# Optimization experiments

Hardware: AMD Instinct MI355X
Metric: run time of the kernel (lower is better)

Reference implementation:

```python
import jax, jax.numpy as jnp
import numpy as np
import math

B, S, E, H = 2, 2048, 1024, 16
D = E // H  # d_head = 64

def setup_inputs() -> dict:
    key = jax.random.key(0)
    ks = jax.random.split(key, 7)
    query = jax.random.normal(ks[0], (B, S, E), dtype=jnp.float32)
    k_in = jax.random.normal(ks[1], (B, S, E), dtype=jnp.float32)
    v_in = jax.random.normal(ks[2], (B, S, E), dtype=jnp.float32)
    # causal mask, broadcastable over batch and heads; mask==0 positions are blocked
    mask = jnp.tril(jnp.ones((S, S), dtype=jnp.int32))[None, None]
    scale = 1.0 / math.sqrt(E)
    w_q = jax.random.normal(ks[3], (E, E), dtype=jnp.float32) * scale
    w_k = jax.random.normal(ks[4], (E, E), dtype=jnp.float32) * scale
    w_v = jax.random.normal(ks[5], (E, E), dtype=jnp.float32) * scale
    w_o = jax.random.normal(ks[6], (E, E), dtype=jnp.float32) * scale
    return {"query": query, "key": k_in, "value": v_in, "mask": mask,
            "w_q": w_q, "w_k": w_k, "w_v": w_v, "w_o": w_o}

def reference(query, key, value, mask, w_q, w_k, w_v, w_o):
    # projections (nn.Linear with no bias: x @ W^T); split heads -> [B,H,S,D]
    q = (query @ w_q.T).reshape(B, S, H, D).transpose(0, 2, 1, 3)
    k = (key @ w_k.T).reshape(B, S, H, D).transpose(0, 2, 1, 3)
    v = (value @ w_v.T).reshape(B, S, H, D).transpose(0, 2, 1, 3)
    # scaled dot-product scores [B,H,S,S]
    scores = jnp.einsum('bhqd,bhkd->bhqk', q, k) / math.sqrt(D)
    scores = jnp.where(mask == 0, jnp.float32(-1e9), scores)
    attn = jax.nn.softmax(scores, axis=-1)  # dropout p=0.0 -> identity
    out = jnp.einsum('bhqk,bhkd->bhqd', attn, v)  # [B,H,S,D]
    out = out.transpose(0, 2, 1, 3).reshape(B, S, E)
    return out @ w_o.T
```

## Files before the change

### kernel.cpp

```cpp
#include <hip/hip_runtime.h>
#include <hip/hip_bf16.h>

#define B_ 2
#define S_ 2048
#define E_ 1024
#define H_ 16
#define D_ 64

typedef __attribute__((ext_vector_type(8))) short bf16x8;
typedef __attribute__((ext_vector_type(4))) float f32x4;

static __device__ __forceinline__ unsigned short f2bf(float x) {
    union { float f; unsigned u; } v; v.f = x;
    unsigned r = v.u + 0x7FFF + ((v.u >> 16) & 1);
    return (unsigned short)(r >> 16);
}

static __device__ __forceinline__ unsigned pack2bf(float a, float b) {
    union { float f; unsigned u; } x, y; x.f = a; y.f = b;
    unsigned ra = x.u + 0x7FFF + ((x.u >> 16) & 1);
    unsigned rb = y.u + 0x7FFF + ((y.u >> 16) & 1);
    return (ra >> 16) | (rb & 0xFFFF0000u);
}

static __device__ __forceinline__ unsigned packtrunc(float a, float b) {
    union { float f; unsigned u; } x, y; x.f = a; y.f = b;
    return __builtin_amdgcn_perm(y.u, x.u, 0x07060302);
}

static __device__ __forceinline__ void async_copy16(const void* gsrc, void* ldst) {
    __builtin_amdgcn_global_load_lds(
        (const __attribute__((address_space(1))) void*)gsrc,
        (__attribute__((address_space(3))) void*)ldst, 16, 0, 0);
}

__global__ void cvt_all(const float* __restrict__ s0, const float* __restrict__ s1,
                        const float* __restrict__ s2, const float* __restrict__ s3,
                        const float* __restrict__ s4, const float* __restrict__ s5,
                        const float* __restrict__ s6,
                        unsigned short* __restrict__ xdst, unsigned short* __restrict__ wdst,
                        float scq) {
    int b = blockIdx.x;
    const float* src; unsigned short* dst; int i; float c = 1.f;
    if (b < 12288) {
        int ti = b >> 12, lb = b & 4095;
        src = (ti == 0) ? s0 : (ti == 1) ? s1 : s2;
        dst = xdst + (size_t)ti * 4194304;
        i = lb * 256 + threadIdx.x;
    } else {
        int r = b - 12288, ti = r >> 10, lb = r & 1023;
        src = (ti == 0) ? s3 : (ti == 1) ? s4 : (ti == 2) ? s5 : s6;
        dst = wdst + (size_t)ti * 1048576;
        i = lb * 256 + threadIdx.x;
        if (ti == 0) c = scq;
    }
    float4 f = ((const float4*)src)[i];
    ushort4 o;
    o.x = f2bf(f.x * c); o.y = f2bf(f.y * c); o.z = f2bf(f.z * c); o.w = f2bf(f.w * c);
    ((ushort4*)dst)[i] = o;
}

template <int MODE>
__global__ __launch_bounds__(256) void gemm128(
    const unsigned short* __restrict__ A0, const unsigned short* __restrict__ B0,
    void* __restrict__ C0, int M, int N, int K) {
    __shared__ __align__(16) unsigned short Al[2][128 * 64];
    __shared__ __align__(16) unsigned short Bl[2][128 * 64];
    const unsigned short* A = A0;
    const unsigned short* Bm = B0;
    int z = 0;
    if (MODE == 4) {
        z = blockIdx.z;
        A  = A0 + (size_t)z * 4194304;
        Bm = B0 + (size_t)z * 1048576;
    }
    const int o = (int)(blockIdx.x + (blockIdx.y << 3));
    const int cx = o & 7, tx = o >> 3;
    const int bm = ((cx << 2) + (tx >> 3)) * 128;
    const int bn = (tx & 7) * 128;
    const int tid = threadIdx.x;
    const int w = tid >> 6, lane = tid & 63;
    const int col = lane & 15, quad = lane >> 4, swz = col & 7;
    const int wm = (w >> 1) * 64, wn = (w & 1) * 64;

    f32x4 acc[4][4] = {};

#pragma unroll
    for (int it = 0; it < 4; it++) {
        int s = tid + it * 256, r = s >> 3, cg = (s & 7) ^ (r & 7);
        async_copy16(A + (size_t)(bm + r) * K + cg * 8, &Al[0][s * 8]);
        async_copy16(Bm + (size_t)(bn + r) * K + cg * 8, &Bl[0][s * 8]);
    }

    const int nk = K >> 6;
    for (int kt = 0; kt < nk; kt++) {
        const int cur = kt & 1;
        __syncthreads();
        if (kt + 1 < nk) {
            const int k1 = (kt + 1) << 6, nb = cur ^ 1;
#pragma unroll
            for (int it = 0; it < 4; it++) {
                int s = tid + it * 256, r = s >> 3, cg = (s & 7) ^ (r & 7);
                async_copy16(A + (size_t)(bm + r) * K + k1 + cg * 8, &Al[nb][s * 8]);
                async_copy16(Bm + (size_t)(bn + r) * K + k1 + cg * 8, &Bl[nb][s * 8]);
            }
        }
        const unsigned short* Ab = &Al[cur][0];
        const unsigned short* Bb = &Bl[cur][0];
#pragma unroll
        for (int h = 0; h < 2; h++) {
            const int cq = ((h * 4 + quad) ^ swz) * 8;
            bf16x8 af[4], bf[4];
#pragma unroll
            for (int i = 0; i < 4; i++) af[i] = *(const bf16x8*)&Ab[(wm + i * 16 + col) * 64 + cq];
#pragma unroll
            for (int j = 0; j < 4; j++) bf[j] = *(const bf16x8*)&Bb[(wn + j * 16 + col) * 64 + cq];
#pragma unroll
            for (int i = 0; i < 4; i++)
#pragma unroll
                for (int j = 0; j < 4; j++)
                    acc[i][j] = __builtin_amdgcn_mfma_f32_16x16x32_bf16(af[i], bf[j], acc[i][j], 0, 0, 0);
        }
    }

    if (MODE == 3) {
#pragma unroll
        for (int i = 0; i < 4; i++)
#pragma unroll
            for (int j = 0; j < 4; j++)
#pragma unroll
                for (int r = 0; r < 4; r++) {
                    int gm = bm + wm + i * 16 + quad * 4 + r;
                    int gn = bn + wn + j * 16 + col;
                    ((float*)C0)[(size_t)gm * N + gn] = acc[i][j][r];
                }
    } else {
        __syncthreads();
        unsigned short* scr = ((w < 2) ? &Al[0][0] : &Bl[0][0]) + (w & 1) * 4096;
        const int b  = (bm + wm) >> 11;
        const int s0 = (bm + wm) & 2047;
        const int hh = (bn + wn) >> 6;
        unsigned short* outp = (unsigned short*)C0 + (size_t)z * 4194304;
        if (z == 2) {
#pragma unroll
            for (int i = 0; i < 4; i++)
#pragma unroll
                for (int j = 0; j < 4; j++) {
                    int n = j * 16 + col;
                    int c = i * 2 + (quad >> 1);
                    uint2 pk;
                    pk.x = pack2bf(acc[i][j][0], acc[i][j][1]);
                    pk.y = pack2bf(acc[i][j][2], acc[i][j][3]);
                    *(uint2*)&scr[n * 64 + ((c ^ (n & 7)) << 3) + ((quad & 1) << 2)] = pk;
                }
#pragma unroll
            for (int it = 0; it < 8; it++) {
                int slot = it * 64 + lane, n = slot >> 3, c = slot & 7;
                uint4 v = *(uint4*)&scr[n * 64 + ((c ^ (n & 7)) << 3)];
                *(uint4*)&outp[(((size_t)b * H_ + hh) * D_ + n) * S_ + s0 + c * 8] = v;
            }
        } else {
#pragma unroll
            for (int i = 0; i < 4; i++)
#pragma unroll
                for (int j = 0; j < 4; j++)
#pragma unroll
                    for (int r = 0; r < 4; r++) {
                        int m = i * 16 + quad * 4 + r, n = j * 16 + col;
                        scr[m * 64 + (((n >> 3) ^ (m & 7)) << 3) + (n & 7)] = f2bf(acc[i][j][r]);
                    }
#pragma unroll
            for (int it = 0; it < 8; it++) {
                int slot = it * 64 + lane, m = slot >> 3, c = slot & 7;
                uint4 v = *(uint4*)&scr[m * 64 + ((c ^ (m & 7)) << 3)];
                *(uint4*)&outp[(((size_t)b * H_ + hh) * S_ + s0 + m) * (size_t)D_ + c * 8] = v;
            }
        }
    }
}

__global__ __launch_bounds__(512) void attn_kernel(
    const unsigned short* __restrict__ Q, const unsigned short* __restrict__ K_,
    const unsigned short* __restrict__ Vt, unsigned short* __restrict__ Out) {
    __shared__ __align__(16) unsigned short KV[4][4096];
    __shared__ __align__(16) float Lred[4][2][64];
    const int o = (int)(blockIdx.x + (blockIdx.y << 4));
    const int cx = o & 7, tx = o >> 3;
    const int bh = (cx << 2) + (tx & 3);
    const int qi = tx >> 2;
    const int qb = (bh >= 16) ? qi : 15 - qi;
    const int q0 = qb * 128;
    const int tid = threadIdx.x;
    const int w = tid >> 6, lane = tid & 63;
    const int qg = w >> 1, kh = w & 1, kh32 = kh << 5;
    const int col = lane & 15, quad = lane >> 4, swz = col & 7;
    const int qw0 = q0 + qg * 32;
    const float NINF = -__builtin_huge_valf();

    const unsigned short* Qh = Q + (size_t)bh * S_ * D_;
    const unsigned short* Kh = K_ + (size_t)bh * S_ * D_;
    const unsigned short* Vh = Vt + (size_t)bh * D_ * S_;

    bf16x8 qf[2][2];
#pragma unroll
    for (int i = 0; i < 2; i++)
#pragma unroll
        for (int h = 0; h < 2; h++)
            qf[i][h] = *(const bf16x8*)(Qh + (size_t)(qw0 + i * 16 + col) * 64 + h * 32 + quad * 8);

    f32x4 o_[2][4] = {};
    float lsum[2] = {0.f, 0.f};

    {
        int s = tid, r = s >> 3, cg = (s & 7) ^ (r & 7);
        async_copy16(Kh + (size_t)r * 64 + cg * 8, &KV[0][s * 8]);
        async_copy16(Vh + (size_t)r * S_ + cg * 8, &KV[2][s * 8]);
    }

    const int nk = 2 * (qb + 1);
    for (int kt = 0; kt < nk; kt++) {
        const int k0 = kt * 64;
        const int cur = kt & 1;
        __syncthreads();
        if (kt + 1 < nk) {
            const int k1 = k0 + 64, nb = cur ^ 1;
            int s = tid, r = s >> 3, cg = (s & 7) ^ (r & 7);
            async_copy16(Kh + (size_t)(k1 + r) * 64 + cg * 8, &KV[nb][s * 8]);
            async_copy16(Vh + (size_t)r * S_ + k1 + cg * 8, &KV[2 + nb][s * 8]);
        }
        if (k0 + kh32 > qw0 + 31) continue;

        const unsigned short* Kb = &KV[cur][0];
        const unsigned short* Vb = &KV[2 + cur][0];

        f32x4 sc[2][2] = {};
#pragma unroll
        for (int h = 0; h < 2; h++) {
            const int cq = ((h * 4 + quad) ^ swz) * 8;
#pragma unroll
            for (int ct = 0; ct < 2; ct++) {
                bf16x8 kf = *(const bf16x8*)&Kb[(kh32 + ct * 16 + col) * 64 + cq];
                sc[0][ct] = __builtin_amdgcn_mfma_f32_16x16x32_bf16(kf, qf[0][h], sc[0][ct], 0, 0, 0);
                sc[1][ct] = __builtin_amdgcn_mfma_f32_16x16x32_bf16(kf, qf[1][h], sc[1][ct], 0, 0, 0);
            }
        }
        if (k0 + kh32 + 31 <= qw0) {
#pragma unroll
            for (int i = 0; i < 2; i++)
#pragma unroll
                for (int ct = 0; ct < 2; ct++) {
#pragma unroll
                    for (int r = 0; r < 4; r++)
                        sc[i][ct][r] = __builtin_amdgcn_exp2f(sc[i][ct][r]);
                    lsum[i] += (sc[i][ct][0] + sc[i][ct][1]) + (sc[i][ct][2] + sc[i][ct][3]);
                }
        } else {
#pragma unroll
            for (int i = 0; i < 2; i++)
#pragma unroll
                for (int ct = 0; ct < 2; ct++) {
#pragma unroll
                    for (int r = 0; r < 4; r++) {
                        int key = k0 + kh32 + ct * 16 + quad * 4 + r;
                        int qidx = qw0 + i * 16 + col;
                        float s = (key <= qidx) ? sc[i][ct][r] : NINF;
                        sc[i][ct][r] = __builtin_amdgcn_exp2f(s);
                    }
                    lsum[i] += (sc[i][ct][0] + sc[i][ct][1]) + (sc[i][ct][2] + sc[i][ct][3]);
                }
        }
        union { bf16x8 v; unsigned u[4]; } pf[2];
#pragma unroll
        for (int i = 0; i < 2; i++) {
            pf[i].u[0] = packtrunc(sc[i][0][0], sc[i][0][1]);
            pf[i].u[1] = packtrunc(sc[i][0][2], sc[i][0][3]);
            pf[i].u[2] = packtrunc(sc[i][1][0], sc[i][1][1]);
            pf[i].u[3] = packtrunc(sc[i][1][2], sc[i][1][3]);
        }
#pragma unroll
        for (int dt = 0; dt < 4; dt++) {
            const int row = dt * 16 + col;
            const int ko0 = kh32 + quad * 4;
            const int ko1 = ko0 + 16;
            union { bf16x8 v; uint2 d2[2]; } vf;
            vf.d2[0] = *(const uint2*)&Vb[row * 64 + (((ko0 >> 3) ^ (row & 7)) << 3) + (ko0 & 7)];
            vf.d2[1] = *(const uint2*)&Vb[row * 64 + (((ko1 >> 3) ^ (row & 7)) << 3) + (ko1 & 7)];
#pragma unroll
            for (int i = 0; i < 2; i++)
                o_[i][dt] = __builtin_amdgcn_mfma_f32_16x16x32_bf16(vf.v, pf[i].v, o_[i][dt], 0, 0, 0);
        }
    }

    __syncthreads();
    if (kh == 1) {
        f32x4* R = (f32x4*)&KV[0][0] + qg * 512 + lane * 8;
#pragma unroll
        for (int i = 0; i < 2; i++)
#pragma unroll
            for (int dt = 0; dt < 4; dt++) R[i * 4 + dt] = o_[i][dt];
        Lred[qg][0][lane] = lsum[0];
        Lred[qg][1][lane] = lsum[1];
    }
    __syncthreads();
    if (kh == 0) {
        f32x4* R = (f32x4*)&KV[0][0] + qg * 512 + lane * 8;
#pragma unroll
        for (int i = 0; i < 2; i++)
#pragma unroll
            for (int dt = 0; dt < 4; dt++) o_[i][dt] += R[i * 4 + dt];
        lsum[0] += Lred[qg][0][lane];
        lsum[1] += Lred[qg][1][lane];

        const int b = bh >> 4, hh = bh & 15;
#pragma unroll
        for (int i = 0; i < 2; i++) {
            float l = lsum[i];
            l += __shfl_xor(l, 16);
            l += __shfl_xor(l, 32);
            float inv = 1.f / l;
            int gq = qw0 + i * 16 + col;
#pragma unroll
            for (int dt = 0; dt < 4; dt++) {
                uint2 pk;
                pk.x = pack2bf(o_[i][dt][0] * inv, o_[i][dt][1] * inv);
                pk.y = pack2bf(o_[i][dt][2] * inv, o_[i][dt][3] * inv);
                *(uint2*)&Out[((size_t)b * S_ + gq) * E_ + hh * 64 + dt * 16 + quad * 4] = pk;
            }
        }
    }
}

extern "C" void kernel_launch(void* const* d_in, const int* in_sizes, int n_in,
                              void* d_out, int out_size, void* d_ws, size_t ws_size,
                              hipStream_t stream) {
    const float* query = (const float*)d_in[0];
    const float* key_i = (const float*)d_in[1];
    const float* value = (const float*)d_in[2];
    const float* w_q = (const float*)d_in[4];
    const float* w_k = (const float*)d_in[5];
    const float* w_v = (const float*)d_in[6];
    const float* w_o = (const float*)d_in[7];
    float* out = (float*)d_out;

    const int M = B_ * S_;
    const int N = E_, K = E_;

    char* ws = (char*)d_ws;
    unsigned short* xq  = (unsigned short*)(ws);
    unsigned short* wqb = (unsigned short*)(ws + (24u << 20));
    unsigned short* Qb  = (unsigned short*)(ws + (32u << 20));
    unsigned short* Kb  = (unsigned short*)(ws + (40u << 20));
    unsigned short* Vtb = (unsigned short*)(ws + (48u << 20));
    unsigned short* Ab  = (unsigned short*)(ws + (56u << 20));

    const float SCQ = 0.125f * 1.44269504088896f;

    cvt_all<<<16384, 256, 0, stream>>>(query, key_i, value, w_q, w_k, w_v, w_o,
                                       xq, wqb, SCQ);

    gemm128<4><<<dim3(N / 128, M / 128, 3), 256, 0, stream>>>(xq, wqb, Qb, M, N, K);

    attn_kernel<<<dim3(S_ / 128, B_ * H_), 512, 0, stream>>>(Qb, Kb, Vtb, Ab);

    gemm128<3><<<dim3(N / 128, M / 128), 256, 0, stream>>>(
        Ab, wqb + 3u * 1048576u, out, M, N, K);
}
```

Baseline: 219.1 us.

## Deepen K/V async prefetch to four-stage ring and remap attention block schedule

Replaces double-buffered K/V shared-memory staging with a four-slot ring that prefetches two tiles ahead, using an explicit vmcnt wait plus a raw barrier instead of __syncthreads. The goal is to hide global-load latency behind more in-flight copies. It also remaps block index to (head, query-block) with a new interleaving that pairs short and long causal rows for load balance. Shared memory usage doubles, which may cut occupancy. The tail issues redundant loads of the last tile so the vmcnt count stays uniform.

```diff
diff --git a/kernel.cpp b/kernel.cpp
--- a/kernel.cpp
+++ b/kernel.cpp
@@ -182,13 +182,15 @@
 __global__ __launch_bounds__(512) void attn_kernel(
     const unsigned short* __restrict__ Q, const unsigned short* __restrict__ K_,
     const unsigned short* __restrict__ Vt, unsigned short* __restrict__ Out) {
-    __shared__ __align__(16) unsigned short KV[4][4096];
+    __shared__ __align__(16) unsigned short KV[8][4096];
     __shared__ __align__(16) float Lred[4][2][64];
     const int o = (int)(blockIdx.x + (blockIdx.y << 4));
     const int cx = o & 7, tx = o >> 3;
-    const int bh = (cx << 2) + (tx & 3);
-    const int qi = tx >> 2;
-    const int qb = (bh >= 16) ? qi : 15 - qi;
+    const int hloc = (tx >> 1) & 3;
+    const int f_ = (tx ^ (tx >> 5)) & 1;
+    const int G_ = (((tx >> 4) & 1) << 2) | (((tx >> 3) & 1) << 1) | (tx & 1);
+    const int qb = f_ ? (G_ ^ 15) : G_;
+    const int bh = (cx << 2) + hloc;
     const int q0 = qb * 128;
     const int tid = threadIdx.x;
     const int w = tid >> 6, lane = tid & 63;
@@ -211,27 +213,34 @@
     f32x4 o_[2][4] = {};
     float lsum[2] = {0.f, 0.f};
 
-    {
-        int s = tid, r = s >> 3, cg = (s & 7) ^ (r & 7);
-        async_copy16(Kh + (size_t)r * 64 + cg * 8, &KV[0][s * 8]);
-        async_copy16(Vh + (size_t)r * S_ + cg * 8, &KV[2][s * 8]);
-    }
+    const int sRow = tid >> 3, sCg = (tid & 7) ^ (sRow & 7);
+    const size_t koff = (size_t)sRow * 64 + sCg * 8;
+    const size_t voff = (size_t)sRow * S_ + sCg * 8;
+    const int ldsoff = tid * 8;
 
     const int nk = 2 * (qb + 1);
+
+    async_copy16(Kh + koff, &KV[0][ldsoff]);
+    async_copy16(Vh + voff, &KV[4][ldsoff]);
+    async_copy16(Kh + koff + 64 * 64, &KV[1][ldsoff]);
+    async_copy16(Vh + voff + 64, &KV[5][ldsoff]);
+
     for (int kt = 0; kt < nk; kt++) {
         const int k0 = kt * 64;
-        const int cur = kt & 1;
-        __syncthreads();
-        if (kt + 1 < nk) {
-            const int k1 = k0 + 64, nb = cur ^ 1;
-            int s = tid, r = s >> 3, cg = (s & 7) ^ (r & 7);
-            async_copy16(Kh + (size_t)(k1 + r) * 64 + cg * 8, &KV[nb][s * 8]);
-            async_copy16(Vh + (size_t)r * S_ + k1 + cg * 8, &KV[2 + nb][s * 8]);
-        }
+        {
+            const int kp = kt + 2;
+            const int src = (kp < nk) ? kp : (nk - 1);
+            const int bp = kp & 3;
+            async_copy16(Kh + koff + (size_t)src * 4096, &KV[bp][ldsoff]);
+            async_copy16(Vh + voff + (size_t)src * 64, &KV[4 + bp][ldsoff]);
+        }
+        asm volatile("s_waitcnt vmcnt(4)" ::: "memory");
+        __builtin_amdgcn_s_barrier();
+
         if (k0 + kh32 > qw0 + 31) continue;
 
-        const unsigned short* Kb = &KV[cur][0];
-        const unsigned short* Vb = &KV[2 + cur][0];
+        const unsigned short* Kb = &KV[kt & 3][0];
+        const unsigned short* Vb = &KV[4 + (kt & 3)][0];
 
         f32x4 sc[2][2] = {};
 #pragma unroll
```

Result: faster. 211.7 us (-3.4%).
